# Performance work log

Measured on AMD Instinct MI355X. Metric: run time of the kernel, lower is better.

## Reference

```python
import jax, jax.numpy as jnp
import numpy as np
import math

B, A, I, O = 4096, 32, 256, 256


def setup_inputs() -> dict:
    key = jax.random.key(0)
    kx, kw, kb = jax.random.split(key, 3)
    x = jax.random.normal(kx, (B, A, I), dtype=jnp.float32)
    # kaiming_uniform_(a=sqrt(5)) on [A, O, I]: fan_in = I, bound = sqrt(6/((1+5)*I)) = 1/sqrt(I)
    wb = 1.0 / math.sqrt(I)
    weight = jax.random.uniform(kw, (A, O, I), minval=-wb, maxval=wb, dtype=jnp.float32)
    bb = 1.0 / math.sqrt(I)
    bias = jax.random.uniform(kb, (A, O), minval=-bb, maxval=bb, dtype=jnp.float32)
    return {"x": x, "weight": weight, "bias": bias}


def reference(x, weight, bias):
    # per-assignment batched GEMM: weight [A,O,I], x [B,A,I] -> [B,A,O]
    return jnp.einsum('aoi,bai->bao', weight, x) + bias
```

## Files before the change

kernel.cpp:

```cpp
#include <hip/hip_runtime.h>

typedef __attribute__((ext_vector_type(4))) float f32x4;
typedef __attribute__((ext_vector_type(2))) unsigned u32x2;
typedef __attribute__((ext_vector_type(8))) short bf16x8;

constexpr int Bsz = 4096, Asz = 32, Isz = 256, Osz = 256;
constexpr int NT = 32;

__device__ inline unsigned cvtpk(float lo, float hi) {
    unsigned r;
    asm("v_cvt_pk_bf16_f32 %0, %1, %2" : "=v"(r) : "v"(lo), "v"(hi));
    return r;
}

__global__ __launch_bounds__(512, 2) void al_gemm(const float* __restrict__ x,
                                                  const float* __restrict__ wsrc,
                                                  const float* __restrict__ bias,
                                                  float* __restrict__ out)
{
    __shared__ char sA[2][8192];
    __shared__ char sB[131072];

    const int p  = blockIdx.x;
    const int a  = (p & 7) * 4 + ((p >> 3) & 3);
    const int b0 = (p >> 5) * 512;

    const int t    = threadIdx.x;
    const int w    = t >> 6;
    const int lane = t & 63;
    const int llo  = lane & 15, lhi = lane >> 4;

    const int lr0 = 2 * w, lr1 = 2 * w + 1;
    const float* fs0 = x + ((size_t)(b0 + lr0) * Asz + a) * Isz + lane * 4;
    const float* fs1 = x + ((size_t)(b0 + lr1) * Asz + a) * Isz + lane * 4;
    const int wa0 = lr0 * 512 + (((lane >> 1) ^ lr0) << 4) + (lane & 1) * 8;
    const int wa1 = lr1 * 512 + (((lane >> 1) ^ lr1) << 4) + (lane & 1) * 8;

    f32x4 L0, L1;
    L0 = *(const f32x4*)fs0;
    L1 = *(const f32x4*)fs1;
    asm volatile("" : "+v"(L0), "+v"(L1));

    {
        const float* wa = wsrc + (size_t)a * (Osz * Isz);
#pragma unroll
        for (int i = 0; i < 16; ++i) {
            const int s     = i * 512 + t;
            const int o     = s >> 5;
            const int kt    = (s >> 2) & 7;
            const int nf    = s >> 9;
            const int lane_ = (o & 15) | ((s & 3) << 4);
            f32x4 lo = *(const f32x4*)(wa + (size_t)s * 8);
            f32x4 hi = *(const f32x4*)(wa + (size_t)s * 8 + 4);
            union { bf16x8 v; unsigned u[4]; } r;
            r.u[0] = cvtpk(lo[0], lo[1]); r.u[1] = cvtpk(lo[2], lo[3]);
            r.u[2] = cvtpk(hi[0], hi[1]); r.u[3] = cvtpk(hi[2], hi[3]);
            *(bf16x8*)&sB[(((kt * 16 + nf) * 64) + lane_) * 16] = r.v;
        }
    }

    const float bv0 = bias[a * Osz + w * 32 + llo];
    const float bv1 = bias[a * Osz + w * 32 + 16 + llo];

    *(u32x2*)&sA[0][wa0] = (u32x2){cvtpk(L0[0], L0[1]), cvtpk(L0[2], L0[3])};
    *(u32x2*)&sA[0][wa1] = (u32x2){cvtpk(L1[0], L1[1]), cvtpk(L1[2], L1[3])};

    __syncthreads();

    for (int tn = 0; tn < NT; ++tn) {
        if (tn < NT - 1) {
            const size_t o_ = (size_t)(tn + 1) * (16 * Asz * Isz);
            L0 = *(const f32x4*)(fs0 + o_);
            L1 = *(const f32x4*)(fs1 + o_);
            asm volatile("" : "+v"(L0), "+v"(L1));
        }

        const char* As = &sA[tn & 1][0];
        f32x4 acc0 = (f32x4)(bv0), acc1 = (f32x4)(bv1);
        __builtin_amdgcn_s_setprio(1);
#pragma unroll
        for (int kt = 0; kt < 8; ++kt) {
            const bf16x8 aF = *(const bf16x8*)&As[llo * 512 + ((((kt * 4) + lhi) ^ llo) << 4)];
            const bf16x8 bF0 = *(const bf16x8*)&sB[(kt * 16 + 2 * w) * 1024 + lane * 16];
            const bf16x8 bF1 = *(const bf16x8*)&sB[(kt * 16 + 2 * w + 1) * 1024 + lane * 16];
            acc0 = __builtin_amdgcn_mfma_f32_16x16x32_bf16(aF, bF0, acc0, 0, 0, 0);
            acc1 = __builtin_amdgcn_mfma_f32_16x16x32_bf16(aF, bF1, acc1, 0, 0, 0);
        }
        __builtin_amdgcn_s_setprio(0);

        const int trow = b0 + tn * 16 + lhi * 4;
        float* op = out + ((size_t)trow * Asz + a) * Osz + w * 32 + llo;
#pragma unroll
        for (int r2 = 0; r2 < 4; ++r2) {
            op[(size_t)r2 * Asz * Osz]      = acc0[r2];
            op[(size_t)r2 * Asz * Osz + 16] = acc1[r2];
        }

        if (tn < NT - 1) {
            char* Ad = &sA[(tn + 1) & 1][0];
            *(u32x2*)&Ad[wa0] = (u32x2){cvtpk(L0[0], L0[1]), cvtpk(L0[2], L0[3])};
            *(u32x2*)&Ad[wa1] = (u32x2){cvtpk(L1[0], L1[1]), cvtpk(L1[2], L1[3])};
        }

        __syncthreads();
    }
}

extern "C" void kernel_launch(void* const* d_in, const int* in_sizes, int n_in,
                              void* d_out, int out_size, void* d_ws, size_t ws_size,
                              hipStream_t stream) {
    const float* x    = (const float*)d_in[0];
    const float* w    = (const float*)d_in[1];
    const float* bias = (const float*)d_in[2];
    float* out        = (float*)d_out;
    al_gemm<<<dim3(256), dim3(512), 0, stream>>>(x, w, bias, out);
}
```

Baseline: 60.18 us.

## Load A fragments directly into registers and compute full-N tiles per wave

Removes the shared-memory staging buffer for x and the per-tile __syncthreads. Each wave now loads its own 16 rows of x straight into MFMA fragment registers, with a 4-deep register prefetch ring. Each wave computes all 16 N-fragments (256 outputs) for its rows instead of 2 fragments across a 16-row tile shared by all waves. This cuts LDS traffic and barriers, but raises register pressure (16 accumulators plus 8 prefetch vectors) and makes each lane's global loads strided across rows.

```diff
diff --git a/kernel.cpp b/kernel.cpp
--- a/kernel.cpp
+++ b/kernel.cpp
@@ -1,11 +1,9 @@
 #include <hip/hip_runtime.h>
 
 typedef __attribute__((ext_vector_type(4))) float f32x4;
-typedef __attribute__((ext_vector_type(2))) unsigned u32x2;
 typedef __attribute__((ext_vector_type(8))) short bf16x8;
 
-constexpr int Bsz = 4096, Asz = 32, Isz = 256, Osz = 256;
-constexpr int NT = 32;
+constexpr int Asz = 32, Isz = 256, Osz = 256;
 
 __device__ inline unsigned cvtpk(float lo, float hi) {
     unsigned r;
@@ -18,7 +16,6 @@
                                                   const float* __restrict__ bias,
                                                   float* __restrict__ out)
 {
-    __shared__ char sA[2][8192];
     __shared__ char sB[131072];
 
     const int p  = blockIdx.x;
@@ -30,16 +27,17 @@
     const int lane = t & 63;
     const int llo  = lane & 15, lhi = lane >> 4;
 
-    const int lr0 = 2 * w, lr1 = 2 * w + 1;
-    const float* fs0 = x + ((size_t)(b0 + lr0) * Asz + a) * Isz + lane * 4;
-    const float* fs1 = x + ((size_t)(b0 + lr1) * Asz + a) * Isz + lane * 4;
-    const int wa0 = lr0 * 512 + (((lane >> 1) ^ lr0) << 4) + (lane & 1) * 8;
-    const int wa1 = lr1 * 512 + (((lane >> 1) ^ lr1) << 4) + (lane & 1) * 8;
+    const float* pA = x + ((size_t)(b0 + w * 16 + llo) * Asz + a) * Isz + lhi * 8;
+    const size_t TSTEP = (size_t)128 * Asz * Isz;
 
-    f32x4 L0, L1;
-    L0 = *(const f32x4*)fs0;
-    L1 = *(const f32x4*)fs1;
-    asm volatile("" : "+v"(L0), "+v"(L1));
+    f32x4 L[4][2];
+
+#define AISSUE(set, off) {                                                     \
+    L[set][0] = *(const f32x4*)(pA + (off));                                   \
+    L[set][1] = *(const f32x4*)(pA + (off) + 4);                               \
+    asm volatile("" : "+v"(L[set][0]), "+v"(L[set][1])); }
+
+    AISSUE(0, 0); AISSUE(1, 32); AISSUE(2, 64); AISSUE(3, 96);
 
     {
         const float* wa = wsrc + (size_t)a * (Osz * Isz);
@@ -59,51 +57,51 @@
         }
     }
 
-    const float bv0 = bias[a * Osz + w * 32 + llo];
-    const float bv1 = bias[a * Osz + w * 32 + 16 + llo];
-
-    *(u32x2*)&sA[0][wa0] = (u32x2){cvtpk(L0[0], L0[1]), cvtpk(L0[2], L0[3])};
-    *(u32x2*)&sA[0][wa1] = (u32x2){cvtpk(L1[0], L1[1]), cvtpk(L1[2], L1[3])};
+    float bv[16];
+#pragma unroll
+    for (int n = 0; n < 16; ++n) bv[n] = bias[a * Osz + n * 16 + llo];
 
     __syncthreads();
 
-    for (int tn = 0; tn < NT; ++tn) {
-        if (tn < NT - 1) {
-            const size_t o_ = (size_t)(tn + 1) * (16 * Asz * Isz);
-            L0 = *(const f32x4*)(fs0 + o_);
-            L1 = *(const f32x4*)(fs1 + o_);
-            asm volatile("" : "+v"(L0), "+v"(L1));
+    for (int tt = 0; tt < 4; ++tt) {
+        f32x4 acc[16];
+#pragma unroll
+        for (int n = 0; n < 16; ++n) acc[n] = (f32x4)(bv[n]);
+
+#pragma unroll
+        for (int kt = 0; kt < 8; ++kt) {
+            const int set = kt & 3;
+            union { bf16x8 v; unsigned u[4]; } r;
+            r.u[0] = cvtpk(L[set][0][0], L[set][0][1]);
+            r.u[1] = cvtpk(L[set][0][2], L[set][0][3]);
+            r.u[2] = cvtpk(L[set][1][0], L[set][1][1]);
+            r.u[3] = cvtpk(L[set][1][2], L[set][1][3]);
+            const bf16x8 aF = r.v;
+
+            if (kt < 4) {
+                AISSUE(set, (size_t)tt * TSTEP + (kt + 4) * 32);
+            } else if (tt < 3) {
+                AISSUE(set, (size_t)(tt + 1) * TSTEP + (kt - 4) * 32);
+            }
+
+            __builtin_amdgcn_s_setprio(1);
+#pragma unroll
+            for (int n = 0; n < 16; ++n) {
+                const bf16x8 bF = *(const bf16x8*)&sB[(kt * 16 + n) * 1024 + lane * 16];
+                acc[n] = __builtin_amdgcn_mfma_f32_16x16x32_bf16(aF, bF, acc[n], 0, 0, 0);
+            }
+            __builtin_amdgcn_s_setprio(0);
         }
 
-        const char* As = &sA[tn & 1][0];
-        f32x4 acc0 = (f32x4)(bv0), acc1 = (f32x4)(bv1);
-        __builtin_amdgcn_s_setprio(1);
+        const int trow = b0 + (tt * 8 + w) * 16 + lhi * 4;
+        float* op = out + ((size_t)trow * Asz + a) * Osz + llo;
 #pragma unroll
-        for (int kt = 0; kt < 8; ++kt) {
-            const bf16x8 aF = *(const bf16x8*)&As[llo * 512 + ((((kt * 4) + lhi) ^ llo) << 4)];
-            const bf16x8 bF0 = *(const bf16x8*)&sB[(kt * 16 + 2 * w) * 1024 + lane * 16];
-            const bf16x8 bF1 = *(const bf16x8*)&sB[(kt * 16 + 2 * w + 1) * 1024 + lane * 16];
-            acc0 = __builtin_amdgcn_mfma_f32_16x16x32_bf16(aF, bF0, acc0, 0, 0, 0);
-            acc1 = __builtin_amdgcn_mfma_f32_16x16x32_bf16(aF, bF1, acc1, 0, 0, 0);
-        }
-        __builtin_amdgcn_s_setprio(0);
-
-        const int trow = b0 + tn * 16 + lhi * 4;
-        float* op = out + ((size_t)trow * Asz + a) * Osz + w * 32 + llo;
+        for (int n = 0; n < 16; ++n)
 #pragma unroll
-        for (int r2 = 0; r2 < 4; ++r2) {
-            op[(size_t)r2 * Asz * Osz]      = acc0[r2];
-            op[(size_t)r2 * Asz * Osz + 16] = acc1[r2];
-        }
-
-        if (tn < NT - 1) {
-            char* Ad = &sA[(tn + 1) & 1][0];
-            *(u32x2*)&Ad[wa0] = (u32x2){cvtpk(L0[0], L0[1]), cvtpk(L0[2], L0[3])};
-            *(u32x2*)&Ad[wa1] = (u32x2){cvtpk(L1[0], L1[1]), cvtpk(L1[2], L1[3])};
-        }
-
-        __syncthreads();
+            for (int r2 = 0; r2 < 4; ++r2)
+                op[(size_t)r2 * Asz * Osz + n * 16] = acc[n][r2];
     }
+#undef AISSUE
 }
 
 extern "C" void kernel_launch(void* const* d_in, const int* in_sizes, int n_in,
```

New measurement: 70.31 us. 1.17x slower.
